# Optimization experiments

Hardware: AMD Instinct MI355X
Metric: run time of the kernel (lower is better)

The kernel has to match this reference:

```python
import jax
import jax.numpy as jnp
import numpy as np

B, N, C_IN, C_OUT, K = 16, 4096, 64, 128, 16
RATIO = 0.25
M = int(RATIO * N)  # 1024 sampled points per cloud
EPS = 1e-5


def setup_inputs() -> dict:
    key = jax.random.key(0)
    ks = jax.random.split(key, 4)
    features = jax.random.normal(ks[0], (B, N, C_IN), dtype=jnp.float32)
    positions = jax.random.normal(ks[1], (B, N, 3), dtype=jnp.float32)
    batch = jnp.repeat(jnp.arange(B, dtype=jnp.int64), N)  # [B*N]
    W = jax.random.normal(ks[2], (C_IN, C_OUT), dtype=jnp.float32) * 0.1
    b = jax.random.normal(ks[3], (C_OUT,), dtype=jnp.float32) * 0.1
    gamma = jnp.ones((C_OUT,), dtype=jnp.float32)
    beta = jnp.zeros((C_OUT,), dtype=jnp.float32)
    return {"features": features, "positions": positions, "batch": batch,
            "W": W, "b": b, "gamma": gamma, "beta": beta}


def _fps_single(pos):
    """Farthest point sampling on one cloud. pos: [N,3] -> indices [M] (start at 0)."""
    def step(carry, _):
        min_d, last = carry
        d = jnp.sum((pos - pos[last]) ** 2, axis=-1)       # [N]
        min_d = jnp.minimum(min_d, d)
        nxt = jnp.argmax(min_d).astype(jnp.int32)
        return (min_d, nxt), nxt
    init = (jnp.full((N,), 1e10, dtype=pos.dtype), jnp.int32(0))
    _, rest = jax.lax.scan(step, init, None, length=M - 1)
    return jnp.concatenate([jnp.zeros((1,), jnp.int32), rest])


def reference(features, positions, batch, W, b, gamma, beta):
    # --- FPS per batch (on positions) ---
    fps_idx = jax.vmap(_fps_single)(positions)                     # [B, M] int32

    # --- MLP: Linear + BatchNorm1d (training-mode batch stats over all B*N points) ---
    h = jnp.einsum('bnc,co->bno', features, W) + b                 # [B, N, C_OUT]
    flat = h.reshape(-1, C_OUT)
    mean = jnp.mean(flat, axis=0)
    var = jnp.mean((flat - mean) ** 2, axis=0)                     # biased, as BN
    hn = (h - mean) * jax.lax.rsqrt(var + EPS) * gamma + beta      # [B, N, C_OUT]

    # --- kNN in FEATURE space: queries = sampled features, keys = all features ---
    q = jnp.take_along_axis(features, fps_idx[..., None], axis=1)  # [B, M, C_IN]
    d2 = (jnp.sum(q * q, -1)[:, :, None]
          + jnp.sum(features * features, -1)[:, None, :]
          - 2.0 * jnp.einsum('bmd,bnd->bmn', q, features))         # [B, M, N]
    _, nbr = jax.lax.top_k(-d2, K)                                 # [B, M, K]

    # --- gather MLP'd features at neighbors, max-pool per sampled point ---
    gathered = jnp.take_along_axis(hn, nbr.reshape(B, M * K)[..., None], axis=1)
    new_features = gathered.reshape(B, M, K, C_OUT).max(axis=2)    # [B, M, C_OUT]

    new_positions = jnp.take_along_axis(positions, fps_idx[..., None], axis=1)  # [B, M, 3]
    new_batch = jnp.take_along_axis(batch.reshape(B, N), fps_idx.astype(jnp.int64), axis=1).reshape(-1)
    return new_features, new_positions, new_batch
```

## Files before the change

### kernel.cpp

```cpp
#include <hip/hip_runtime.h>

#define B_ 16
#define N_ 4096
#define CIN_ 64
#define COUT_ 128
#define K_ 16
#define M_ 1024

typedef float f32x2 __attribute__((ext_vector_type(2)));
typedef unsigned long long u64;

#define DPPF(m, ctrl)                                                          \
  m = fmaxf(m, __int_as_float(__builtin_amdgcn_update_dpp(                     \
                  0, __float_as_int(m), ctrl, 0xF, 0xF, true)))
#define DPPI(e, ctrl)                                                          \
  e = max(e, __builtin_amdgcn_update_dpp(0, e, ctrl, 0xF, 0xF, true))

__device__ __forceinline__ unsigned mono32(float d) {
  unsigned u = __float_as_uint(d);
  return u ^ (unsigned)(((int)u >> 31) | 0x80000000);
}

__device__ __forceinline__ unsigned short f2bf(float x) {
  const unsigned u = __float_as_uint(x);
  return (unsigned short)((u + 0x7FFF + ((u >> 16) & 1)) >> 16);
}
__device__ __forceinline__ float bf2f(unsigned short s) {
  return __uint_as_float((unsigned)s << 16);
}

__global__ __launch_bounds__(512) void mega_kernel(
    const float* __restrict__ pos, const float* __restrict__ features,
    const float* __restrict__ W, const float* __restrict__ bias,
    int* __restrict__ fps_idx, unsigned short* __restrict__ h,
    float* __restrict__ stats, int* __restrict__ prog,
    u64* __restrict__ cand, int S) {
  __shared__ __align__(16) char smem[84 * 1024];
  const int id = blockIdx.x;
  const int t = threadIdx.x;

  if (id < B_) {
    const int b = id;
    float4* P = (float4*)smem;
    volatile u64* red = (volatile u64*)(smem + 65536);
    const float* pb = pos + (size_t)b * N_ * 3;
    if (t < 8) ((u64*)(smem + 65536))[t] = 0;
    for (int i = t; i < N_; i += 512)
      P[i] = make_float4(pb[i * 3], pb[i * 3 + 1], pb[i * 3 + 2], 0.f);
    __syncthreads();
    if (t >= 256) return;
    f32x2 px[8], py[8], pz[8], md[8];
#pragma unroll
    for (int j = 0; j < 8; ++j) {
      const float4 lo = P[t + 512 * j];
      const float4 hi = P[t + 512 * j + 256];
      px[j] = (f32x2){lo.x, hi.x};
      py[j] = (f32x2){lo.y, hi.y};
      pz[j] = (f32x2){lo.z, hi.z};
      md[j] = (f32x2){1e10f, 1e10f};
    }
    if (t == 0) fps_idx[b * M_] = 0;
    const int wv = t >> 6, ln = t & 63;
    const int e0 = 65535 - t;
    float4 lp = P[0];
    for (int step = 1; step < M_; ++step) {
      const f32x2 lx = {lp.x, lp.x}, ly = {lp.y, lp.y}, lz = {lp.z, lp.z};
      float bestd = -1.0f;
      int be = 0;
      {
#pragma clang fp contract(off)
#pragma unroll
        for (int j = 0; j < 8; ++j) {
          const f32x2 dx = px[j] - lx;
          const f32x2 dy = py[j] - ly;
          const f32x2 dz = pz[j] - lz;
          const f32x2 s1 = dx * dx;
          const f32x2 s2 = dy * dy;
          const f32x2 s3 = dz * dz;
          const f32x2 d = (s1 + s2) + s3;
          f32x2 nd;
          nd.x = fminf(md[j].x, d.x);
          nd.y = fminf(md[j].y, d.y);
          md[j] = nd;
          if (nd.x > bestd) { bestd = nd.x; be = e0 - (j << 9); }
          if (nd.y > bestd) { bestd = nd.y; be = e0 - (j << 9) - 256; }
        }
      }
      float m = bestd;
      DPPF(m, 0x111); DPPF(m, 0x112); DPPF(m, 0x114); DPPF(m, 0x118);
      DPPF(m, 0x142); DPPF(m, 0x143);
      const float wm =
          __int_as_float(__builtin_amdgcn_readlane(__float_as_int(m), 63));
      int enc = (bestd == wm) ? be : 0;
      DPPI(enc, 0x111); DPPI(enc, 0x112); DPPI(enc, 0x114); DPPI(enc, 0x118);
      DPPI(enc, 0x142); DPPI(enc, 0x143);
      const int wenc = __builtin_amdgcn_readlane(enc, 63);
      const unsigned tag = (unsigned)(step & 1023);
      volatile u64* rb = red + (step & 1) * 4;
      if (ln == 0)
        rb[wv] = ((u64)__float_as_uint(wm) << 32) | ((u64)tag << 16) |
                 (unsigned)wenc;
      u64 r0, r1, r2, r3;
      for (;;) {
        r0 = rb[0]; r1 = rb[1]; r2 = rb[2]; r3 = rb[3];
        const u64 x = ((r0 >> 16) ^ tag) | ((r1 >> 16) ^ tag) |
                      ((r2 >> 16) ^ tag) | ((r3 >> 16) ^ tag);
        if (!(x & 0x3FF)) break;
      }
      u64 rr = r0 > r1 ? r0 : r1;
      const u64 rc = r2 > r3 ? r2 : r3;
      if (rc > rr) rr = rc;
      const int last = 65535 - (int)(unsigned)(rr & 0xFFFFu);
      lp = P[last];
      if (t == 0) {
        fps_idx[b * M_ + step] = last;
        if ((step & 63) == 63)
          __hip_atomic_store(&prog[b], (step >> 6) + 1, __ATOMIC_RELEASE,
                             __HIP_MEMORY_SCOPE_AGENT);
      }
    }
    return;
  }

  if (id < B_ + 512) {
    const int lid = id - B_;
    float* ls = (float*)smem;
    for (int i = t; i < 256; i += 512) ls[i] = 0.f;
    __syncthreads();
    const int o4 = (t & 31) << 2;
    const int rl = t >> 5;
    const float4 bv = *(const float4*)(bias + o4);
    float4 s4 = {0, 0, 0, 0}, ss4 = {0, 0, 0, 0};
    for (int i = 0; i < 8; ++i) {
      const int r = lid * 128 + rl * 8 + i;
      const float4* fr = (const float4*)(features + (size_t)r * CIN_);
      float4 acc = bv;
#pragma unroll
      for (int c4 = 0; c4 < 16; ++c4) {
        const float4 fv = fr[c4];
        const float* wr = W + (size_t)(c4 * 4) * COUT_ + o4;
        const float4 w0 = *(const float4*)(wr);
        const float4 w1 = *(const float4*)(wr + COUT_);
        const float4 w2 = *(const float4*)(wr + 2 * COUT_);
        const float4 w3 = *(const float4*)(wr + 3 * COUT_);
        acc.x = fmaf(fv.x, w0.x, acc.x); acc.y = fmaf(fv.x, w0.y, acc.y);
        acc.z = fmaf(fv.x, w0.z, acc.z); acc.w = fmaf(fv.x, w0.w, acc.w);
        acc.x = fmaf(fv.y, w1.x, acc.x); acc.y = fmaf(fv.y, w1.y, acc.y);
        acc.z = fmaf(fv.y, w1.z, acc.z); acc.w = fmaf(fv.y, w1.w, acc.w);
        acc.x = fmaf(fv.z, w2.x, acc.x); acc.y = fmaf(fv.z, w2.y, acc.y);
        acc.z = fmaf(fv.z, w2.z, acc.z); acc.w = fmaf(fv.z, w2.w, acc.w);
        acc.x = fmaf(fv.w, w3.x, acc.x); acc.y = fmaf(fv.w, w3.y, acc.y);
        acc.z = fmaf(fv.w, w3.z, acc.z); acc.w = fmaf(fv.w, w3.w, acc.w);
      }
      *(ushort4*)(h + (size_t)r * COUT_ + o4) =
          make_ushort4(f2bf(acc.x), f2bf(acc.y), f2bf(acc.z), f2bf(acc.w));
      s4.x += acc.x; s4.y += acc.y; s4.z += acc.z; s4.w += acc.w;
      ss4.x = fmaf(acc.x, acc.x, ss4.x); ss4.y = fmaf(acc.y, acc.y, ss4.y);
      ss4.z = fmaf(acc.z, acc.z, ss4.z); ss4.w = fmaf(acc.w, acc.w, ss4.w);
    }
    atomicAdd(&ls[o4 + 0], s4.x); atomicAdd(&ls[o4 + 1], s4.y);
    atomicAdd(&ls[o4 + 2], s4.z); atomicAdd(&ls[o4 + 3], s4.w);
    atomicAdd(&ls[128 + o4 + 0], ss4.x); atomicAdd(&ls[128 + o4 + 1], ss4.y);
    atomicAdd(&ls[128 + o4 + 2], ss4.z); atomicAdd(&ls[128 + o4 + 3], ss4.w);
    __syncthreads();
    if (t < 128) {
      atomicAdd(&stats[t], ls[t]);
      atomicAdd(&stats[128 + t], ls[128 + t]);
    }
    return;
  }

  {
    const int kid = id - (B_ + 512);
    const int qt = kid / (B_ * S);
    const int rem = kid % (B_ * S);
    const int b = rem / S;
    const int s = rem % S;
    const int KPS = N_ / S;
    const int KT = KPS / 128;
    float* Qs = (float*)smem;
    float* Ks = (float*)(smem + 16384);
    float* sd2 = (float*)(smem + 49152);
    float* qq = (float*)(smem + 82944);
    float* ff = (float*)(smem + 83200);
    int* qid = (int*)(smem + 83712);
    const float* fb = features + (size_t)b * N_ * CIN_;

    if (t == 0) {
      while (__hip_atomic_load(&prog[b], __ATOMIC_ACQUIRE,
                               __HIP_MEMORY_SCOPE_AGENT) < qt + 1)
        __builtin_amdgcn_s_sleep(16);
    }
    __syncthreads();
    if (t < 64) qid[t] = fps_idx[b * M_ + qt * 64 + t];
    __syncthreads();
#pragma unroll
    for (int st = 0; st < 2; ++st) {
      const int iid = t + 512 * st;
      const int row = iid >> 4, c4 = iid & 15;
      const int pc = (c4 + (row >> 2)) & 15;
      const float4 v = *(const float4*)(fb + (size_t)qid[row] * CIN_ + c4 * 4);
      *(float4*)(&Qs[row * 64 + pc * 4]) = v;
    }
    __syncthreads();
    if (t < 64) {
      float sv = 0.f;
#pragma unroll
      for (int c4 = 0; c4 < 16; ++c4) {
        const int pc = (c4 + (t >> 2)) & 15;
        const float4 v = *(const float4*)(&Qs[t * 64 + pc * 4]);
        sv = fmaf(v.x, v.x, sv); sv = fmaf(v.y, v.y, sv);
        sv = fmaf(v.z, v.z, sv); sv = fmaf(v.w, v.w, sv);
      }
      qq[t] = sv;
    }

    u64 lst[16];
#pragma unroll
    for (int p = 0; p < 16; ++p) lst[p] = ~0ull;
    u64 worst = ~0ull;
    int wpos = 0;

    const int q0 = (t >> 5) * 4;
    const int k0 = (t & 31) * 4;
    const int sq = t >> 3;
    const int ssub = t & 7;

    for (int kt = 0; kt < KT; ++kt) {
      const int kb = s * KPS + kt * 128;
#pragma unroll
      for (int st = 0; st < 4; ++st) {
        const int iid = t + 512 * st;
        const int row = iid >> 4, c4 = iid & 15;
        const int pc = (c4 + (row >> 2)) & 15;
        const float4 v =
            *(const float4*)(fb + (size_t)(kb + row) * CIN_ + c4 * 4);
        *(float4*)(&Ks[row * 64 + pc * 4]) = v;
      }
      __syncthreads();
      if (t < 128) {
        float sv = 0.f;
#pragma unroll
        for (int c4 = 0; c4 < 16; ++c4) {
          const int pc = (c4 + (t >> 2)) & 15;
          const float4 v = *(const float4*)(&Ks[t * 64 + pc * 4]);
          sv = fmaf(v.x, v.x, sv); sv = fmaf(v.y, v.y, sv);
          sv = fmaf(v.z, v.z, sv); sv = fmaf(v.w, v.w, sv);
        }
        ff[t] = sv;
      }
      __syncthreads();
      float acc[4][4];
#pragma unroll
      for (int i = 0; i < 4; ++i)
#pragma unroll
        for (int j = 0; j < 4; ++j) acc[i][j] = 0.f;
#pragma unroll
      for (int c4 = 0; c4 < 16; ++c4) {
        float4 qv[4], kv[4];
#pragma unroll
        for (int i = 0; i < 4; ++i) {
          const int row = q0 + i;
          const int pc = (c4 + (row >> 2)) & 15;
          qv[i] = *(const float4*)(&Qs[row * 64 + pc * 4]);
        }
#pragma unroll
        for (int j = 0; j < 4; ++j) {
          const int row = k0 + j;
          const int pc = (c4 + (row >> 2)) & 15;
          kv[j] = *(const float4*)(&Ks[row * 64 + pc * 4]);
        }
#pragma unroll
        for (int i = 0; i < 4; ++i)
#pragma unroll
          for (int j = 0; j < 4; ++j) {
            acc[i][j] = fmaf(qv[i].x, kv[j].x, acc[i][j]);
            acc[i][j] = fmaf(qv[i].y, kv[j].y, acc[i][j]);
            acc[i][j] = fmaf(qv[i].z, kv[j].z, acc[i][j]);
            acc[i][j] = fmaf(qv[i].w, kv[j].w, acc[i][j]);
          }
      }
#pragma unroll
      for (int i = 0; i < 4; ++i) {
        const float qv = qq[q0 + i];
        float4 o;
        o.x = __fsub_rn(__fadd_rn(qv, ff[k0 + 0]), 2.f * acc[i][0]);
        o.y = __fsub_rn(__fadd_rn(qv, ff[k0 + 1]), 2.f * acc[i][1]);
        o.z = __fsub_rn(__fadd_rn(qv, ff[k0 + 2]), 2.f * acc[i][2]);
        o.w = __fsub_rn(__fadd_rn(qv, ff[k0 + 3]), 2.f * acc[i][3]);
        *(float4*)(&sd2[(q0 + i) * 132 + k0]) = o;
      }
      __syncthreads();
#pragma unroll
      for (int g = 0; g < 4; ++g) {
        const float4 v = *(const float4*)(&sd2[sq * 132 + ssub * 16 + g * 4]);
        const float dv[4] = {v.x, v.y, v.z, v.w};
#pragma unroll
        for (int jj = 0; jj < 4; ++jj) {
          const int key = kb + ssub * 16 + g * 4 + jj;
          const u64 pk = ((u64)mono32(dv[jj]) << 32) | (unsigned)key;
          if (pk < worst) {
#pragma unroll
            for (int p = 0; p < 16; ++p)
              if (p == wpos) lst[p] = pk;
            worst = lst[0]; wpos = 0;
#pragma unroll
            for (int p = 1; p < 16; ++p)
              if (lst[p] > worst) { worst = lst[p]; wpos = p; }
          }
        }
      }
      __syncthreads();
    }
    u64* cb = cand + ((size_t)(b * M_ + qt * 64 + sq) * S + s) * 16;
    for (int r = 0; r < K_; ++r) {
      u64 mn = lst[0];
#pragma unroll
      for (int p = 1; p < 16; ++p)
        if (lst[p] < mn) mn = lst[p];
      u64 m2 = mn;
#pragma unroll
      for (int off = 1; off < 8; off <<= 1) {
        const u64 o = __shfl_xor(m2, off, 64);
        if (o < m2) m2 = o;
      }
      if (mn == m2) {
        bool done = false;
#pragma unroll
        for (int p = 0; p < 16; ++p)
          if (!done && lst[p] == m2) { lst[p] = ~0ull; done = true; }
      }
      if (ssub == 0) cb[r] = m2;
    }
  }
}

__global__ void finalize_kernel(float* __restrict__ stats,
                                const float* __restrict__ gamma,
                                const float* __restrict__ beta) {
  const int o = threadIdx.x;
  const float inv = 1.0f / (float)(B_ * N_);
  const float mean = stats[o] * inv;
  const float var = stats[128 + o] * inv - mean * mean;
  const float r = 1.0f / sqrtf(var + 1e-5f);
  const float sc = gamma[o] * r;
  stats[256 + o] = sc;
  stats[384 + o] = beta[o] - mean * sc;
}

__global__ __launch_bounds__(256) void gather_kernel(
    const unsigned short* __restrict__ h, const float* __restrict__ stats,
    const u64* __restrict__ cand, float* __restrict__ out, int S) {
  const int g = blockIdx.x;
  const int t = threadIdx.x;
  const int S16 = S * 16;
  __shared__ u64 cl[2][128];
  __shared__ int nbi[32];
  const int Q0 = g * 2;
  if (t < 2 * S16) {
    const int qi = t / S16, sl = t % S16;
    cl[qi][sl] = cand[(size_t)(Q0 + qi) * S16 + sl];
  }
  __syncthreads();
  if ((t & 127) == 0) {
    const int qi = t >> 7;
    int ptr[8] = {0, 0, 0, 0, 0, 0, 0, 0};
    for (int r = 0; r < K_; ++r) {
      u64 mn = ~0ull;
      int ms = 0;
      for (int s = 0; s < S; ++s) {
        if (ptr[s] < 16) {
          const u64 v = cl[qi][s * 16 + ptr[s]];
          if (v < mn) { mn = v; ms = s; }
        }
      }
      nbi[qi * 16 + r] = (int)(unsigned)(mn & 0xFFFFFFFFu);
      ptr[ms]++;
    }
  }
  __syncthreads();
  const int q2 = t >> 7, o = t & 127;
  const int Q = Q0 + q2, b = Q >> 10;
  const float sc = stats[256 + o];
  const float sh = stats[384 + o];
  float mx = -3.402823466e38f;
#pragma unroll
  for (int k = 0; k < K_; ++k) {
    const int n = nbi[q2 * 16 + k];
    const float v = fmaf(bf2f(h[((size_t)b * N_ + n) * COUT_ + o]), sc, sh);
    mx = fmaxf(mx, v);
  }
  out[(size_t)Q * COUT_ + o] = mx;
}

__global__ __launch_bounds__(256) void tail_kernel(const float* __restrict__ pos,
                                                   const int* __restrict__ fps_idx,
                                                   float* __restrict__ out,
                                                   int batch_as_i64) {
  const int gid = blockIdx.x * 256 + threadIdx.x;
  const int A = B_ * M_ * COUT_;
  const int P = B_ * M_ * 3;
  if (gid < P) {
    const int Q = gid / 3;
    const int c = gid - Q * 3;
    const int b = Q >> 10;
    const int idx = fps_idx[Q];
    out[A + gid] = pos[((size_t)b * N_ + idx) * 3 + c];
  } else {
    const int Q = gid - P;
    if (Q < B_ * M_) {
      const int b = Q >> 10;
      float* base = out + A + P;
      if (batch_as_i64)
        ((long long*)base)[Q] = (long long)b;
      else
        base[Q] = (float)b;
    }
  }
}

extern "C" void kernel_launch(void* const* d_in, const int* in_sizes, int n_in,
                              void* d_out, int out_size, void* d_ws, size_t ws_size,
                              hipStream_t stream) {
  const float* features = (const float*)d_in[0];
  const float* positions = (const float*)d_in[1];
  const float* W = (const float*)d_in[3];
  const float* bias = (const float*)d_in[4];
  const float* gamma = (const float*)d_in[5];
  const float* beta = (const float*)d_in[6];
  float* out = (float*)d_out;
  unsigned char* ws = (unsigned char*)d_ws;

  int* fps_idx = (int*)ws;
  unsigned short* h = (unsigned short*)(ws + 65536);
  const size_t hoff = 65536 + (size_t)B_ * N_ * COUT_ * 2;
  float* stats = (float*)(ws + hoff);
  int* prog = (int*)(ws + hoff + 2048);
  u64* cand = (u64*)(ws + hoff + 2048 + 256);
  const size_t base = hoff + 2048 + 256;

  int S = 8;
  while (S > 1 && base + (size_t)B_ * M_ * S * 16 * 8 > ws_size) S >>= 1;

  const int rem = out_size - (B_ * M_ * COUT_) - (B_ * M_ * 3);
  const int batch_as_i64 = (rem >= 2 * B_ * M_) ? 1 : 0;

  hipMemsetAsync(stats, 0, 2048 + 256, stream);
  mega_kernel<<<B_ + 512 + 256 * S, 512, 0, stream>>>(
      positions, features, W, bias, fps_idx, h, stats, prog, cand, S);
  finalize_kernel<<<1, 128, 0, stream>>>(stats, gamma, beta);
  gather_kernel<<<B_ * M_ / 2, 256, 0, stream>>>(h, stats, cand, out, S);
  tail_kernel<<<256, 256, 0, stream>>>(positions, fps_idx, out, batch_as_i64);
}
```

Baseline: 1.043 ms.

## Use persistent ticket-based kNN workers and fuse finalize, gather and tail kernels

```diff
diff --git a/kernel.cpp b/kernel.cpp
--- a/kernel.cpp
+++ b/kernel.cpp
@@ -20,24 +20,22 @@
   unsigned u = __float_as_uint(d);
   return u ^ (unsigned)(((int)u >> 31) | 0x80000000);
 }
-
 __device__ __forceinline__ unsigned short f2bf(float x) {
   const unsigned u = __float_as_uint(x);
   return (unsigned short)((u + 0x7FFF + ((u >> 16) & 1)) >> 16);
 }
-__device__ __forceinline__ float bf2f(unsigned short s) {
-  return __uint_as_float((unsigned)s << 16);
-}
 
 __global__ __launch_bounds__(512) void mega_kernel(
     const float* __restrict__ pos, const float* __restrict__ features,
     const float* __restrict__ W, const float* __restrict__ bias,
     int* __restrict__ fps_idx, unsigned short* __restrict__ h,
-    float* __restrict__ stats, int* __restrict__ prog,
-    u64* __restrict__ cand, int S) {
+    float* __restrict__ ctrl, u64* __restrict__ cand, int S) {
   __shared__ __align__(16) char smem[84 * 1024];
   const int id = blockIdx.x;
   const int t = threadIdx.x;
+  float* stats = ctrl;
+  int* prog = (int*)(ctrl + 512);
+  int* tickets = (int*)(ctrl + 528);
 
   if (id < B_) {
     const int b = id;
@@ -108,8 +106,8 @@
         if (!(x & 0x3FF)) break;
       }
       u64 rr = r0 > r1 ? r0 : r1;
-      const u64 rc = r2 > r3 ? r2 : r3;
-      if (rc > rr) rr = rc;
+      const u64 r2m = r2 > r3 ? r2 : r3;
+      if (r2m > rr) rr = r2m;
       const int last = 65535 - (int)(unsigned)(rr & 0xFFFFu);
       lp = P[last];
       if (t == 0) {
@@ -171,251 +169,281 @@
   }
 
   {
-    const int kid = id - (B_ + 512);
-    const int qt = kid / (B_ * S);
-    const int rem = kid % (B_ * S);
-    const int b = rem / S;
-    const int s = rem % S;
-    const int KPS = N_ / S;
-    const int KT = KPS / 128;
     float* Qs = (float*)smem;
     float* Ks = (float*)(smem + 16384);
     float* sd2 = (float*)(smem + 49152);
     float* qq = (float*)(smem + 82944);
     float* ff = (float*)(smem + 83200);
     int* qid = (int*)(smem + 83712);
-    const float* fb = features + (size_t)b * N_ * CIN_;
-
-    if (t == 0) {
-      while (__hip_atomic_load(&prog[b], __ATOMIC_ACQUIRE,
-                               __HIP_MEMORY_SCOPE_AGENT) < qt + 1)
-        __builtin_amdgcn_s_sleep(16);
-    }
-    __syncthreads();
-    if (t < 64) qid[t] = fps_idx[b * M_ + qt * 64 + t];
-    __syncthreads();
-#pragma unroll
-    for (int st = 0; st < 2; ++st) {
-      const int iid = t + 512 * st;
-      const int row = iid >> 4, c4 = iid & 15;
-      const int pc = (c4 + (row >> 2)) & 15;
-      const float4 v = *(const float4*)(fb + (size_t)qid[row] * CIN_ + c4 * 4);
-      *(float4*)(&Qs[row * 64 + pc * 4]) = v;
-    }
-    __syncthreads();
-    if (t < 64) {
-      float sv = 0.f;
-#pragma unroll
-      for (int c4 = 0; c4 < 16; ++c4) {
-        const int pc = (c4 + (t >> 2)) & 15;
-        const float4 v = *(const float4*)(&Qs[t * 64 + pc * 4]);
-        sv = fmaf(v.x, v.x, sv); sv = fmaf(v.y, v.y, sv);
-        sv = fmaf(v.z, v.z, sv); sv = fmaf(v.w, v.w, sv);
-      }
-      qq[t] = sv;
-    }
-
-    u64 lst[16];
-#pragma unroll
-    for (int p = 0; p < 16; ++p) lst[p] = ~0ull;
-    u64 worst = ~0ull;
-    int wpos = 0;
-
+    int* tk = (int*)(smem + 83968);
+    const int NT = 256 * S;
     const int q0 = (t >> 5) * 4;
     const int k0 = (t & 31) * 4;
     const int sq = t >> 3;
     const int ssub = t & 7;
-
-    for (int kt = 0; kt < KT; ++kt) {
-      const int kb = s * KPS + kt * 128;
-#pragma unroll
-      for (int st = 0; st < 4; ++st) {
+    const int KPS = N_ / S;
+    const int KT = KPS / 128;
+
+    for (;;) {
+      if (t == 0)
+        *tk = __hip_atomic_fetch_add(tickets, 1, __ATOMIC_RELAXED,
+                                     __HIP_MEMORY_SCOPE_AGENT);
+      __syncthreads();
+      const int ticket = *tk;
+      if (ticket >= NT) return;
+      const int qt = ticket / (B_ * S);
+      const int rem = ticket % (B_ * S);
+      const int b = rem / S;
+      const int s = rem % S;
+      const float* fb = features + (size_t)b * N_ * CIN_;
+
+      if (t == 0) {
+        while (__hip_atomic_load(&prog[b], __ATOMIC_ACQUIRE,
+                                 __HIP_MEMORY_SCOPE_AGENT) < qt + 1)
+          __builtin_amdgcn_s_sleep(16);
+      }
+      __syncthreads();
+      if (t < 64) qid[t] = fps_idx[b * M_ + qt * 64 + t];
+      __syncthreads();
+#pragma unroll
+      for (int st = 0; st < 2; ++st) {
         const int iid = t + 512 * st;
         const int row = iid >> 4, c4 = iid & 15;
         const int pc = (c4 + (row >> 2)) & 15;
-        const float4 v =
-            *(const float4*)(fb + (size_t)(kb + row) * CIN_ + c4 * 4);
-        *(float4*)(&Ks[row * 64 + pc * 4]) = v;
+        const float4 v = *(const float4*)(fb + (size_t)qid[row] * CIN_ + c4 * 4);
+        *(float4*)(&Qs[row * 64 + pc * 4]) = v;
       }
       __syncthreads();
-      if (t < 128) {
+      if (t < 64) {
         float sv = 0.f;
 #pragma unroll
         for (int c4 = 0; c4 < 16; ++c4) {
           const int pc = (c4 + (t >> 2)) & 15;
-          const float4 v = *(const float4*)(&Ks[t * 64 + pc * 4]);
+          const float4 v = *(const float4*)(&Qs[t * 64 + pc * 4]);
           sv = fmaf(v.x, v.x, sv); sv = fmaf(v.y, v.y, sv);
           sv = fmaf(v.z, v.z, sv); sv = fmaf(v.w, v.w, sv);
         }
-        ff[t] = sv;
-      }
-      __syncthreads();
-      float acc[4][4];
-#pragma unroll
-      for (int i = 0; i < 4; ++i)
-#pragma unroll
-        for (int j = 0; j < 4; ++j) acc[i][j] = 0.f;
-#pragma unroll
-      for (int c4 = 0; c4 < 16; ++c4) {
-        float4 qv[4], kv[4];
+        qq[t] = sv;
+      }
+
+      u64 lst[16];
+#pragma unroll
+      for (int p = 0; p < 16; ++p) lst[p] = ~0ull;
+      u64 worst = ~0ull;
+      int wpos = 0;
+
+      for (int kt = 0; kt < KT; ++kt) {
+        const int kb = s * KPS + kt * 128;
+#pragma unroll
+        for (int st = 0; st < 4; ++st) {
+          const int iid = t + 512 * st;
+          const int row = iid >> 4, c4 = iid & 15;
+          const int pc = (c4 + (row >> 2)) & 15;
+          const float4 v =
+              *(const float4*)(fb + (size_t)(kb + row) * CIN_ + c4 * 4);
+          *(float4*)(&Ks[row * 64 + pc * 4]) = v;
+        }
+        __syncthreads();
+        if (t < 128) {
+          float sv = 0.f;
+#pragma unroll
+          for (int c4 = 0; c4 < 16; ++c4) {
+            const int pc = (c4 + (t >> 2)) & 15;
+            const float4 v = *(const float4*)(&Ks[t * 64 + pc * 4]);
+            sv = fmaf(v.x, v.x, sv); sv = fmaf(v.y, v.y, sv);
+            sv = fmaf(v.z, v.z, sv); sv = fmaf(v.w, v.w, sv);
+          }
+          ff[t] = sv;
+        }
+        __syncthreads();
+        float acc[4][4];
+#pragma unroll
+        for (int i = 0; i < 4; ++i)
+#pragma unroll
+          for (int j = 0; j < 4; ++j) acc[i][j] = 0.f;
+#pragma unroll
+        for (int c4 = 0; c4 < 16; ++c4) {
+          float4 qv[4], kv[4];
+#pragma unroll
+          for (int i = 0; i < 4; ++i) {
+            const int row = q0 + i;
+            const int pc = (c4 + (row >> 2)) & 15;
+            qv[i] = *(const float4*)(&Qs[row * 64 + pc * 4]);
+          }
+#pragma unroll
+          for (int j = 0; j < 4; ++j) {
+            const int row = k0 + j;
+            const int pc = (c4 + (row >> 2)) & 15;
+            kv[j] = *(const float4*)(&Ks[row * 64 + pc * 4]);
+          }
+#pragma unroll
+          for (int i = 0; i < 4; ++i)
+#pragma unroll
+            for (int j = 0; j < 4; ++j) {
+              acc[i][j] = fmaf(qv[i].x, kv[j].x, acc[i][j]);
+              acc[i][j] = fmaf(qv[i].y, kv[j].y, acc[i][j]);
+              acc[i][j] = fmaf(qv[i].z, kv[j].z, acc[i][j]);
+              acc[i][j] = fmaf(qv[i].w, kv[j].w, acc[i][j]);
+            }
+        }
 #pragma unroll
         for (int i = 0; i < 4; ++i) {
-          const int row = q0 + i;
-          const int pc = (c4 + (row >> 2)) & 15;
-          qv[i] = *(const float4*)(&Qs[row * 64 + pc * 4]);
-        }
-#pragma unroll
-        for (int j = 0; j < 4; ++j) {
-          const int row = k0 + j;
-          const int pc = (c4 + (row >> 2)) & 15;
-          kv[j] = *(const float4*)(&Ks[row * 64 + pc * 4]);
-        }
-#pragma unroll
-        for (int i = 0; i < 4; ++i)
-#pragma unroll
-          for (int j = 0; j < 4; ++j) {
-            acc[i][j] = fmaf(qv[i].x, kv[j].x, acc[i][j]);
-            acc[i][j] = fmaf(qv[i].y, kv[j].y, acc[i][j]);
-            acc[i][j] = fmaf(qv[i].z, kv[j].z, acc[i][j]);
-            acc[i][j] = fmaf(qv[i].w, kv[j].w, acc[i][j]);
+          const float qv = qq[q0 + i];
+          float4 o;
+          o.x = __fsub_rn(__fadd_rn(qv, ff[k0 + 0]), 2.f * acc[i][0]);
+          o.y = __fsub_rn(__fadd_rn(qv, ff[k0 + 1]), 2.f * acc[i][1]);
+          o.z = __fsub_rn(__fadd_rn(qv, ff[k0 + 2]), 2.f * acc[i][2]);
+          o.w = __fsub_rn(__fadd_rn(qv, ff[k0 + 3]), 2.f * acc[i][3]);
+          *(float4*)(&sd2[(q0 + i) * 132 + k0]) = o;
+        }
+        __syncthreads();
+#pragma unroll
+        for (int g = 0; g < 4; ++g) {
+          const float4 v = *(const float4*)(&sd2[sq * 132 + ssub * 16 + g * 4]);
+          const float dv[4] = {v.x, v.y, v.z, v.w};
+#pragma unroll
+          for (int jj = 0; jj < 4; ++jj) {
+            const int key = kb + ssub * 16 + g * 4 + jj;
+            const u64 pk = ((u64)mono32(dv[jj]) << 32) | (unsigned)key;
+            if (pk < worst) {
+#pragma unroll
+              for (int p = 0; p < 16; ++p)
+                if (p == wpos) lst[p] = pk;
+              worst = lst[0]; wpos = 0;
+#pragma unroll
+              for (int p = 1; p < 16; ++p)
+                if (lst[p] > worst) { worst = lst[p]; wpos = p; }
+            }
           }
-      }
-#pragma unroll
-      for (int i = 0; i < 4; ++i) {
-        const float qv = qq[q0 + i];
-        float4 o;
-        o.x = __fsub_rn(__fadd_rn(qv, ff[k0 + 0]), 2.f * acc[i][0]);
-        o.y = __fsub_rn(__fadd_rn(qv, ff[k0 + 1]), 2.f * acc[i][1]);
-        o.z = __fsub_rn(__fadd_rn(qv, ff[k0 + 2]), 2.f * acc[i][2]);
-        o.w = __fsub_rn(__fadd_rn(qv, ff[k0 + 3]), 2.f * acc[i][3]);
-        *(float4*)(&sd2[(q0 + i) * 132 + k0]) = o;
-      }
-      __syncthreads();
-#pragma unroll
-      for (int g = 0; g < 4; ++g) {
-        const float4 v = *(const float4*)(&sd2[sq * 132 + ssub * 16 + g * 4]);
-        const float dv[4] = {v.x, v.y, v.z, v.w};
-#pragma unroll
-        for (int jj = 0; jj < 4; ++jj) {
-          const int key = kb + ssub * 16 + g * 4 + jj;
-          const u64 pk = ((u64)mono32(dv[jj]) << 32) | (unsigned)key;
-          if (pk < worst) {
-#pragma unroll
-            for (int p = 0; p < 16; ++p)
-              if (p == wpos) lst[p] = pk;
-            worst = lst[0]; wpos = 0;
-#pragma unroll
-            for (int p = 1; p < 16; ++p)
-              if (lst[p] > worst) { worst = lst[p]; wpos = p; }
-          }
-        }
-      }
-      __syncthreads();
-    }
-    u64* cb = cand + ((size_t)(b * M_ + qt * 64 + sq) * S + s) * 16;
-    for (int r = 0; r < K_; ++r) {
-      u64 mn = lst[0];
-#pragma unroll
-      for (int p = 1; p < 16; ++p)
-        if (lst[p] < mn) mn = lst[p];
-      u64 m2 = mn;
-#pragma unroll
-      for (int off = 1; off < 8; off <<= 1) {
-        const u64 o = __shfl_xor(m2, off, 64);
-        if (o < m2) m2 = o;
-      }
-      if (mn == m2) {
-        bool done = false;
-#pragma unroll
-        for (int p = 0; p < 16; ++p)
-          if (!done && lst[p] == m2) { lst[p] = ~0ull; done = true; }
-      }
-      if (ssub == 0) cb[r] = m2;
+        }
+        __syncthreads();
+      }
+      u64* cb = cand + ((size_t)(b * M_ + qt * 64 + sq) * S + s) * 16;
+      for (int r = 0; r < K_; ++r) {
+        u64 mn = lst[0];
+#pragma unroll
+        for (int p = 1; p < 16; ++p)
+          if (lst[p] < mn) mn = lst[p];
+        u64 m2 = mn;
+#pragma unroll
+        for (int off = 1; off < 8; off <<= 1) {
+          const u64 o = __shfl_xor(m2, off, 64);
+          if (o < m2) m2 = o;
+        }
+        if (mn == m2) {
+          bool done = false;
+#pragma unroll
+          for (int p = 0; p < 16; ++p)
+            if (!done && lst[p] == m2) { lst[p] = ~0ull; done = true; }
+        }
+        if (ssub == 0) cb[r] = m2;
+      }
     }
   }
 }
 
-__global__ void finalize_kernel(float* __restrict__ stats,
-                                const float* __restrict__ gamma,
-                                const float* __restrict__ beta) {
-  const int o = threadIdx.x;
-  const float inv = 1.0f / (float)(B_ * N_);
-  const float mean = stats[o] * inv;
-  const float var = stats[128 + o] * inv - mean * mean;
-  const float r = 1.0f / sqrtf(var + 1e-5f);
-  const float sc = gamma[o] * r;
-  stats[256 + o] = sc;
-  stats[384 + o] = beta[o] - mean * sc;
-}
-
-__global__ __launch_bounds__(256) void gather_kernel(
-    const unsigned short* __restrict__ h, const float* __restrict__ stats,
-    const u64* __restrict__ cand, float* __restrict__ out, int S) {
+__global__ __launch_bounds__(256) void gather_tail_kernel(
+    const float* __restrict__ pos, const int* __restrict__ fps_idx,
+    const unsigned short* __restrict__ h, const float* __restrict__ ctrl,
+    const float* __restrict__ gamma, const float* __restrict__ beta,
+    const u64* __restrict__ cand, float* __restrict__ out, int S,
+    int batch_as_i64) {
   const int g = blockIdx.x;
   const int t = threadIdx.x;
+  const int A = B_ * M_ * COUT_;
+  const int P = B_ * M_ * 3;
+  if (g >= 256) {
+    const int gid2 = (g - 256) * 256 + t;
+    for (int i = 0; i < 16; ++i) {
+      const int gid = gid2 + 4096 * i;
+      if (gid < P) {
+        const int Q = gid / 3;
+        const int c = gid - Q * 3;
+        const int b = Q >> 10;
+        const int idx = fps_idx[Q];
+        out[A + gid] = pos[((size_t)b * N_ + idx) * 3 + c];
+      } else {
+        const int Q = gid - P;
+        if (Q < B_ * M_) {
+          const int b = Q >> 10;
+          float* base = out + A + P;
+          if (batch_as_i64)
+            ((long long*)base)[Q] = (long long)b;
+          else
+            base[Q] = (float)b;
+        }
+      }
+    }
+    return;
+  }
+  __shared__ u64 cl[64 * 128];
+  __shared__ int nbi[64 * 16];
+  __shared__ float scsh[256];
+  const int b = g >> 4, qt = g & 15;
+  if (t < 128) {
+    const float inv = 1.0f / (float)(B_ * N_);
+    const float mean = ctrl[t] * inv;
+    const float var = ctrl[128 + t] * inv - mean * mean;
+    const float r = 1.0f / sqrtf(var + 1e-5f);
+    const float sc = gamma[t] * r;
+    scsh[t] = sc;
+    scsh[128 + t] = beta[t] - mean * sc;
+  }
   const int S16 = S * 16;
-  __shared__ u64 cl[2][128];
-  __shared__ int nbi[32];
-  const int Q0 = g * 2;
-  if (t < 2 * S16) {
-    const int qi = t / S16, sl = t % S16;
-    cl[qi][sl] = cand[(size_t)(Q0 + qi) * S16 + sl];
-  }
+  const u64* cg = cand + (size_t)(b * M_ + qt * 64) * S16;
+  for (int i = t; i < 64 * S16; i += 256) cl[i] = cg[i];
   __syncthreads();
-  if ((t & 127) == 0) {
-    const int qi = t >> 7;
+  if (t < 64) {
     int ptr[8] = {0, 0, 0, 0, 0, 0, 0, 0};
     for (int r = 0; r < K_; ++r) {
       u64 mn = ~0ull;
       int ms = 0;
       for (int s = 0; s < S; ++s) {
         if (ptr[s] < 16) {
-          const u64 v = cl[qi][s * 16 + ptr[s]];
+          const u64 v = cl[t * S16 + s * 16 + ptr[s]];
           if (v < mn) { mn = v; ms = s; }
         }
       }
-      nbi[qi * 16 + r] = (int)(unsigned)(mn & 0xFFFFFFFFu);
+      nbi[t * 16 + r] = (int)(unsigned)(mn & 0xFFFFFFFFu);
       ptr[ms]++;
     }
   }
   __syncthreads();
-  const int q2 = t >> 7, o = t & 127;
-  const int Q = Q0 + q2, b = Q >> 10;
-  const float sc = stats[256 + o];
-  const float sh = stats[384 + o];
-  float mx = -3.402823466e38f;
+  const int q = t >> 2;
+  const int c0 = (t & 3) * 32;
+  float mx[32], mn[32];
+#pragma unroll
+  for (int i = 0; i < 32; ++i) { mx[i] = -3.402823466e38f; mn[i] = 3.402823466e38f; }
 #pragma unroll
   for (int k = 0; k < K_; ++k) {
-    const int n = nbi[q2 * 16 + k];
-    const float v = fmaf(bf2f(h[((size_t)b * N_ + n) * COUT_ + o]), sc, sh);
-    mx = fmaxf(mx, v);
-  }
-  out[(size_t)Q * COUT_ + o] = mx;
-}
-
-__global__ __launch_bounds__(256) void tail_kernel(const float* __restrict__ pos,
-                                                   const int* __restrict__ fps_idx,
-                                                   float* __restrict__ out,
-                                                   int batch_as_i64) {
-  const int gid = blockIdx.x * 256 + threadIdx.x;
-  const int A = B_ * M_ * COUT_;
-  const int P = B_ * M_ * 3;
-  if (gid < P) {
-    const int Q = gid / 3;
-    const int c = gid - Q * 3;
-    const int b = Q >> 10;
-    const int idx = fps_idx[Q];
-    out[A + gid] = pos[((size_t)b * N_ + idx) * 3 + c];
-  } else {
-    const int Q = gid - P;
-    if (Q < B_ * M_) {
-      const int b = Q >> 10;
-      float* base = out + A + P;
-      if (batch_as_i64)
-        ((long long*)base)[Q] = (long long)b;
-      else
-        base[Q] = (float)b;
-    }
+    const int n = nbi[q * 16 + k];
+    const uint4* hr = (const uint4*)(h + ((size_t)b * N_ + n) * COUT_ + c0);
+#pragma unroll
+    for (int j = 0; j < 4; ++j) {
+      const uint4 hv = hr[j];
+      const unsigned hu[4] = {hv.x, hv.y, hv.z, hv.w};
+#pragma unroll
+      for (int i = 0; i < 4; ++i) {
+        const float lo = __uint_as_float(hu[i] << 16);
+        const float hi = __uint_as_float(hu[i] & 0xFFFF0000u);
+        const int c = j * 8 + 2 * i;
+        mx[c] = fmaxf(mx[c], lo); mn[c] = fminf(mn[c], lo);
+        mx[c + 1] = fmaxf(mx[c + 1], hi); mn[c + 1] = fminf(mn[c + 1], hi);
+      }
+    }
+  }
+  float* ob = out + (size_t)(b * M_ + qt * 64 + q) * COUT_ + c0;
+#pragma unroll
+  for (int i = 0; i < 8; ++i) {
+    float4 o;
+#pragma unroll
+    for (int e = 0; e < 4; ++e) {
+      const int c = 4 * i + e;
+      const float sc = scsh[c0 + c], sh = scsh[128 + c0 + c];
+      const float v = sc >= 0.f ? mx[c] : mn[c];
+      (&o.x)[e] = fmaf(v, sc, sh);
+    }
+    *(float4*)(ob + 4 * i) = o;
   }
 }
 
@@ -434,10 +462,9 @@
   int* fps_idx = (int*)ws;
   unsigned short* h = (unsigned short*)(ws + 65536);
   const size_t hoff = 65536 + (size_t)B_ * N_ * COUT_ * 2;
-  float* stats = (float*)(ws + hoff);
-  int* prog = (int*)(ws + hoff + 2048);
-  u64* cand = (u64*)(ws + hoff + 2048 + 256);
-  const size_t base = hoff + 2048 + 256;
+  float* ctrl = (float*)(ws + hoff);
+  u64* cand = (u64*)(ws + hoff + 4096);
+  const size_t base = hoff + 4096;
 
   int S = 8;
   while (S > 1 && base + (size_t)B_ * M_ * S * 16 * 8 > ws_size) S >>= 1;
@@ -445,10 +472,9 @@
   const int rem = out_size - (B_ * M_ * COUT_) - (B_ * M_ * 3);
   const int batch_as_i64 = (rem >= 2 * B_ * M_) ? 1 : 0;
 
-  hipMemsetAsync(stats, 0, 2048 + 256, stream);
-  mega_kernel<<<B_ + 512 + 256 * S, 512, 0, stream>>>(
-      positions, features, W, bias, fps_idx, h, stats, prog, cand, S);
-  finalize_kernel<<<1, 128, 0, stream>>>(stats, gamma, beta);
-  gather_kernel<<<B_ * M_ / 2, 256, 0, stream>>>(h, stats, cand, out, S);
-  tail_kernel<<<256, 256, 0, stream>>>(positions, fps_idx, out, batch_as_i64);
+  hipMemsetAsync(ctrl, 0, 4096, stream);
+  mega_kernel<<<B_ + 512 + 240, 512, 0, stream>>>(
+      positions, features, W, bias, fps_idx, h, ctrl, cand, S);
+  gather_tail_kernel<<<256 + 16, 256, 0, stream>>>(
+      positions, fps_idx, h, ctrl, gamma, beta, cand, out, S, batch_as_i64);
 }
```

Result: slower. 1.081 ms (+3.6%).
